# Kernel tuning notes

Hardware: AMD Instinct MI355X
Metric: run time of the kernel (lower is better)

## Reference

```python
import jax, jax.numpy as jnp
import numpy as np

B, C, H, W = 16, 256, 96, 96
K = 3
K2 = K * K


def setup_inputs() -> dict:
    key = jax.random.key(0)
    ks = jax.random.split(key, 8)
    s = 1.0 / np.sqrt(C)  # fan-in style scale for 1x1 convs
    sk = 1.0 / np.sqrt(K2)
    return {
        "x": jax.random.normal(ks[0], (B, C, H, W), jnp.float32),
        "w_xproj": jax.random.normal(ks[1], (C, C), jnp.float32) * s,
        "b_xproj": jnp.zeros((C,), jnp.float32),
        "w_proj": jax.random.normal(ks[2], (C, C), jnp.float32) * s,
        "b_proj": jnp.zeros((C,), jnp.float32),
        "w_kp": jax.random.normal(ks[3], (C, C), jnp.float32) * s,
        "b_kp": jnp.zeros((C,), jnp.float32),
        "w_kg": jax.random.normal(ks[4], (K2, K2), jnp.float32) * sk,
        "b_kg": jnp.zeros((K2,), jnp.float32),
        "diff_ctrl": jnp.zeros((1, 1, 1, C), jnp.float32),
    }


def reference(x, w_xproj, b_xproj, w_proj, b_proj, w_kp, b_kp, w_kg, b_kg, diff_ctrl):
    b, c, h, w = x.shape
    # --- kernel synthesis ---
    # 1x1 conv (kernel_proj)
    kp = jnp.einsum('bchw,oc->bohw', x, w_kp) + b_kp[None, :, None, None]
    # AdaptiveAvgPool1d over flattened spatial dim -> 9 bins (H*W divisible by 9)
    pooled = kp.reshape(b, c, K2, (h * w) // K2).mean(axis=-1)  # [B, C, 9]
    pooled = jax.nn.gelu(pooled)
    # per-channel Linear(9 -> 9): y = W @ v + b
    ker = jnp.einsum('bck,jk->bcj', pooled, w_kg) + b_kg  # [B, C, 9]
    # rearrange 'c (k1 k2) -> k1 k2 1 c' (batched)
    ker = ker.reshape(b, c, K, K).transpose(0, 2, 3, 1)[:, :, :, None, :]  # [B, K, K, 1, C]
    # lateral inhibition: subtract learned fraction of per-channel kernel mean
    factor = jax.nn.sigmoid(diff_ctrl)  # [1, 1, 1, C]
    ker = ker - factor * ker.mean(axis=(1, 2, 3), keepdims=True)
    # --- main path ---
    xp = jnp.einsum('bchw,oc->bohw', x, w_xproj) + b_xproj[None, :, None, None]
    pad = K // 2

    def dwconv(xi, ki):  # xi [C,H,W], ki [K,K,1,C]
        return jax.lax.conv_general_dilated(
            xi[None], ki, window_strides=(1, 1),
            padding=((pad, pad), (pad, pad)),
            dimension_numbers=('NCHW', 'HWIO', 'NCHW'),
            feature_group_count=c)[0]

    y = jax.vmap(dwconv)(xp, ker)  # per-sample dynamic depthwise conv
    out = jnp.einsum('bchw,oc->bohw', y, w_proj) + b_proj[None, :, None, None]
    return out
```

## Files before the change

### kernel.cpp

```cpp
#include <hip/hip_runtime.h>

#define CCH 256
#define HWP 9216
#define IMGDIM 96

typedef __attribute__((ext_vector_type(8))) short s16x8;
typedef __attribute__((ext_vector_type(4))) float f32x4;

__device__ __forceinline__ unsigned short f2bf(float f){
  unsigned u = __float_as_uint(f);
  u += 0x7fffu + ((u >> 16) & 1u);
  return (unsigned short)(u >> 16);
}
__device__ __forceinline__ float bf2f(unsigned short h){
  return __uint_as_float(((unsigned)h) << 16);
}

__global__ void k0_convert(const float* __restrict__ wx, const float* __restrict__ wp,
                           unsigned short* __restrict__ wxb, unsigned short* __restrict__ wpb){
  int i = blockIdx.x * 256 + threadIdx.x;
  wxb[i] = f2bf(wx[i]);
  wpb[i] = f2bf(wp[i]);
}

__device__ __forceinline__ void wload(const unsigned short* __restrict__ wbf,
                                      int obase, int c0, int g, int r, s16x8 wf[8]){
  #pragma unroll
  for (int kk = 0; kk < 2; ++kk){
    #pragma unroll
    for (int mf = 0; mf < 4; ++mf)
      wf[kk*4+mf] = *(const s16x8*)(wbf + (size_t)(obase + mf*16 + r)*CCH + c0 + kk*32 + g*8);
  }
}
__device__ __forceinline__ void gemm_chunk_w(const unsigned short* buf, const s16x8 wf[8],
                                             f32x4 acc[4][4], int g, int r){
  #pragma unroll
  for (int kk = 0; kk < 2; ++kk){
    const int kc = kk*32 + g*8;
    s16x8 bfr[4];
    #pragma unroll
    for (int nf = 0; nf < 4; ++nf){
      const int p = nf*16 + r;
      unsigned off = (unsigned)(p*128 + kc*2) ^ ((unsigned)(p & 7) << 4);
      bfr[nf] = *(const s16x8*)((const char*)buf + off);
    }
    #pragma unroll
    for (int mf = 0; mf < 4; ++mf){
      #pragma unroll
      for (int nf = 0; nf < 4; ++nf){
        acc[mf][nf] = __builtin_amdgcn_mfma_f32_16x16x32_bf16(wf[kk*4+mf], bfr[nf], acc[mf][nf], 0, 0, 0);
      }
    }
  }
}

__device__ __forceinline__ void k1_load(const float* __restrict__ xb, int p0, int c0,
                                        int pg, int cgl, float v[4][4]){
  #pragma unroll
  for (int ci = 0; ci < 4; ++ci){
    float4 q = *(const float4*)(xb + (size_t)(c0 + cgl*4 + ci)*HWP + p0 + pg*4);
    v[ci][0]=q.x; v[ci][1]=q.y; v[ci][2]=q.z; v[ci][3]=q.w;
  }
}
__device__ __forceinline__ void k1_store(unsigned short* buf, int pg, int cgl, float v[4][4],
                                         float* __restrict__ xpart, int c0, int lane, int bbase){
  #pragma unroll
  for (int pj = 0; pj < 4; ++pj){
    const int p = pg*4 + pj;
    unsigned off = (unsigned)(p*128 + cgl*8) ^ ((unsigned)(p & 7) << 4);
    ushort4 pk;
    pk.x = f2bf(v[0][pj]); pk.y = f2bf(v[1][pj]);
    pk.z = f2bf(v[2][pj]); pk.w = f2bf(v[3][pj]);
    *(ushort4*)((char*)buf + off) = pk;
  }
  #pragma unroll
  for (int ci = 0; ci < 4; ++ci){
    float s = v[ci][0] + v[ci][1] + v[ci][2] + v[ci][3];
    s += __shfl_xor(s, 1); s += __shfl_xor(s, 2);
    s += __shfl_xor(s, 4); s += __shfl_xor(s, 8);
    if ((lane & 15) == 0) xpart[bbase + c0 + cgl*4 + ci] = s;
  }
}

__global__ __launch_bounds__(256) void k1_xproj(const float* __restrict__ x,
    const unsigned short* __restrict__ wxb, const float* __restrict__ bx,
    unsigned short* __restrict__ xp, float* __restrict__ xpart){
  const int tile = blockIdx.x, b = blockIdx.y;
  const int p0 = tile * 64;
  const int t = threadIdx.x, lane = t & 63, wave = t >> 6;
  const int g = lane >> 4, r = lane & 15;
  __shared__ __align__(16) unsigned short xlds[2][64*64];

  const float* xb = x + (size_t)b * CCH * HWP;
  const int binj = p0 >> 10, blk = (p0 >> 6) & 15;
  const int bbase = (((int)b*9 + binj)*16 + blk)*CCH;
  const int pg = t & 15, cgl = t >> 4;

  float v[4][4][4];
  s16x8 wf[2][8];
  f32x4 acc[4][4];
  f32x4 zz = {0.f,0.f,0.f,0.f};
  #pragma unroll
  for (int i2=0;i2<4;++i2){
    #pragma unroll
    for (int j2=0;j2<4;++j2) acc[i2][j2] = zz;
  }

  #pragma unroll
  for (int ch = 0; ch < 4; ++ch) k1_load(xb, p0, ch*64, pg, cgl, v[ch]);
  wload(wxb, wave*64, 0, g, r, wf[0]);
  k1_store(xlds[0], pg, cgl, v[0], xpart, 0, lane, bbase);

  #pragma unroll
  for (int ch = 0; ch < 4; ++ch){
    __syncthreads();
    if (ch < 3) wload(wxb, wave*64, (ch+1)*64, g, r, wf[(ch+1)&1]);
    gemm_chunk_w(xlds[ch & 1], wf[ch & 1], acc, g, r);
    if (ch < 3) k1_store(xlds[(ch+1)&1], pg, cgl, v[ch+1], xpart, (ch+1)*64, lane, bbase);
  }

  unsigned short* eb = &xlds[0][0];
  #pragma unroll
  for (int h = 0; h < 2; ++h){
    __syncthreads();
    if ((wave >> 1) == h){
      const int mw = wave & 1;
      #pragma unroll
      for (int mf = 0; mf < 4; ++mf){
        const int o  = mw*64 + mf*16 + 4*g;
        const int og = h*128 + o;
        float b0 = bx[og], b1 = bx[og+1], b2 = bx[og+2], b3 = bx[og+3];
        #pragma unroll
        for (int nf = 0; nf < 4; ++nf){
          const int p = nf*16 + r;
          unsigned off = (unsigned)(p*256 + o*2) ^ ((unsigned)(p & 7) << 4);
          ushort4 pk;
          pk.x = f2bf(acc[mf][nf][0] + b0);
          pk.y = f2bf(acc[mf][nf][1] + b1);
          pk.z = f2bf(acc[mf][nf][2] + b2);
          pk.w = f2bf(acc[mf][nf][3] + b3);
          *(ushort4*)((char*)eb + off) = pk;
        }
      }
    }
    __syncthreads();
    const size_t gb = ((size_t)b*HWP + p0)*CCH + h*128;
    #pragma unroll
    for (int it = 0; it < 4; ++it){
      const unsigned u = it*256 + t;
      const unsigned p = u >> 4, unit = u & 15;
      const unsigned srcoff = (u*16u) ^ ((p & 7) << 4);
      uint4 val = *(const uint4*)((const char*)eb + srcoff);
      *(uint4*)(xp + gb + (size_t)p*CCH + unit*8) = val;
    }
  }
}

__global__ __launch_bounds__(256) void k2a_pooled(const float* __restrict__ xpart,
    const float* __restrict__ wkp, const float* __restrict__ bkp,
    float* __restrict__ pooledg){
  const int j = blockIdx.x, b = blockIdx.y, t = threadIdx.x;
  __shared__ float xbar[256];
  __shared__ float wch[256][65];
  const float* xp0 = xpart + (((size_t)b*9 + j)*16)*CCH;
  float s = 0.f;
  #pragma unroll
  for (int blk = 0; blk < 16; ++blk) s += xp0[blk*CCH + t];
  xbar[t] = s * (1.0f/1024.0f);
  float acc = bkp[t];
  for (int ch = 0; ch < 4; ++ch){
    __syncthreads();
    for (int u = t; u < 256*64; u += 256){
      wch[u >> 6][u & 63] = wkp[(size_t)(u >> 6)*CCH + ch*64 + (u & 63)];
    }
    __syncthreads();
    #pragma unroll
    for (int c = 0; c < 64; ++c) acc += wch[t][c] * xbar[ch*64 + c];
  }
  float x3 = acc*acc*acc;
  float tg = tanhf(0.7978845608028654f*(acc + 0.044715f*x3));
  pooledg[((size_t)b*9 + j)*CCH + t] = 0.5f*acc*(1.0f + tg);
}

__global__ void k2b_ker(const float* __restrict__ pooledg, const float* __restrict__ wkg,
                        const float* __restrict__ bkg, const float* __restrict__ dctrl,
                        float* __restrict__ kerg){
  const int b = blockIdx.x, c = threadIdx.x;
  float pl[9];
  #pragma unroll
  for (int k = 0; k < 9; ++k) pl[k] = pooledg[((size_t)b*9 + k)*CCH + c];
  float kv[9]; float m = 0.f;
  #pragma unroll
  for (int jp = 0; jp < 9; ++jp){
    float s2 = bkg[jp];
    #pragma unroll
    for (int k = 0; k < 9; ++k) s2 += pl[k] * wkg[jp*9 + k];
    kv[jp] = s2; m += s2;
  }
  m *= (1.0f/9.0f);
  float f = 1.0f / (1.0f + expf(-dctrl[c]));
  #pragma unroll
  for (int jp = 0; jp < 9; ++jp) kerg[((size_t)b*9 + jp)*CCH + c] = kv[jp] - f*m;
}

__global__ __launch_bounds__(256) void k3f_conv(const unsigned short* __restrict__ xp,
    const unsigned short* __restrict__ wpb, const float* __restrict__ bp,
    const float* __restrict__ kerg, float* __restrict__ out){
  const int tile = blockIdx.x, b = blockIdx.y;
  const int th0 = (tile / 12) * 8, tw0 = (tile % 12) * 8;
  const int t = threadIdx.x, lane = t & 63, wave = t >> 6;
  const int g = lane >> 4, r = lane & 15;
  __shared__ __align__(16) unsigned short halo[2][100*64];
  __shared__ __align__(16) unsigned short ylds[2][64*64];
  __shared__ __align__(16) float kl[9][256];

  for (int u = t; u < 9*256; u += 256)
    kl[u >> 8][u & 255] = kerg[((size_t)b*9 + (u >> 8))*CCH + (u & 255)];

  const unsigned short* xpb = xp + (size_t)b * HWP * CCH;
  const int p = t >> 2, dh = p >> 3, dw = p & 7, q = t & 3;

  uint4 sreg[4];
  s16x8 wf[2][8];
  f32x4 acc[4][4];
  f32x4 zz = {0.f,0.f,0.f,0.f};
  #pragma unroll
  for (int i2=0;i2<4;++i2){
    #pragma unroll
    for (int j2=0;j2<4;++j2) acc[i2][j2] = zz;
  }

  #define K3F_ISSUE(CH)                                                        \
    _Pragma("unroll")                                                          \
    for (int i = 0; i < 4; ++i){                                               \
      const int u = i*256 + t;                                                 \
      if (u < 800){                                                            \
        const int pos = u >> 3, w8 = u & 7;                                    \
        const int rr = pos / 10, cc = pos % 10;                                \
        const int hh = th0 + rr - 1, ww = tw0 + cc - 1;                        \
        uint4 val = {0u,0u,0u,0u};                                             \
        if (hh >= 0 && hh < IMGDIM && ww >= 0 && ww < IMGDIM)                  \
          val = *(const uint4*)(xpb + ((size_t)(hh*IMGDIM + ww))*CCH + (CH)*64 + w8*8); \
        sreg[i] = val;                                                         \
      }                                                                        \
    }
  #define K3F_WRITE(BUF)                                                       \
    _Pragma("unroll")                                                          \
    for (int i = 0; i < 4; ++i){                                               \
      const int u = i*256 + t;                                                 \
      if (u < 800){                                                            \
        const int pos = u >> 3, w8 = u & 7;                                    \
        unsigned off = (unsigned)(pos*128 + w8*16) ^ ((unsigned)(pos & 7) << 4); \
        *(uint4*)((char*)halo[BUF] + off) = sreg[i];                           \
      }                                                                        \
    }

  wload(wpb, wave*64, 0, g, r, wf[0]);
  K3F_ISSUE(0)
  K3F_WRITE(0)
  __syncthreads();

  #pragma unroll
  for (int ch = 0; ch < 4; ++ch){
    if (ch < 3) K3F_ISSUE(ch+1)
    if (ch > 0) gemm_chunk_w(ylds[(ch-1)&1], wf[(ch-1)&1], acc, g, r);
    if (ch < 3) wload(wpb, wave*64, (ch+1)*64, g, r, wf[(ch+1)&1]);
    #pragma unroll
    for (int ci = 0; ci < 2; ++ci){
      const int c = q*16 + ci*8;
      const int cg = ch*64 + c;
      float a8[8] = {0,0,0,0,0,0,0,0};
      #pragma unroll
      for (int tap = 0; tap < 9; ++tap){
        const int pos = (dh + tap/3)*10 + (dw + tap%3);
        unsigned hof = (unsigned)(pos*128 + c*2) ^ ((unsigned)(pos & 7) << 4);
        union { uint4 qv; unsigned short u16[8]; } hv;
        hv.qv = *(const uint4*)((const char*)halo[ch & 1] + hof);
        const float4* kp4 = (const float4*)&kl[tap][cg];
        float4 ka = kp4[0], kb = kp4[1];
        a8[0] += bf2f(hv.u16[0]) * ka.x;
        a8[1] += bf2f(hv.u16[1]) * ka.y;
        a8[2] += bf2f(hv.u16[2]) * ka.z;
        a8[3] += bf2f(hv.u16[3]) * ka.w;
        a8[4] += bf2f(hv.u16[4]) * kb.x;
        a8[5] += bf2f(hv.u16[5]) * kb.y;
        a8[6] += bf2f(hv.u16[6]) * kb.z;
        a8[7] += bf2f(hv.u16[7]) * kb.w;
      }
      unsigned pk[4];
      #pragma unroll
      for (int e = 0; e < 4; ++e)
        pk[e] = (unsigned)f2bf(a8[2*e]) | ((unsigned)f2bf(a8[2*e+1]) << 16);
      unsigned yoff = (unsigned)(p*128 + c*2) ^ ((unsigned)(p & 7) << 4);
      *(uint4*)((char*)ylds[ch & 1] + yoff) = *(uint4*)pk;
    }
    if (ch < 3) K3F_WRITE((ch+1)&1)
    __syncthreads();
  }
  #undef K3F_ISSUE
  #undef K3F_WRITE

  gemm_chunk_w(ylds[1], wf[1], acc, g, r);

  #pragma unroll
  for (int mf = 0; mf < 4; ++mf){
    const int o = wave*64 + mf*16 + 4*g;
    float b0 = bp[o], b1 = bp[o+1], b2 = bp[o+2], b3 = bp[o+3];
    #pragma unroll
    for (int nf = 0; nf < 4; ++nf){
      const int pl2 = nf*16 + r;
      const int hh = th0 + (pl2 >> 3), ww = tw0 + (pl2 & 7);
      const size_t pix = (size_t)hh*IMGDIM + ww;
      out[((size_t)b*CCH + o + 0)*HWP + pix] = acc[mf][nf][0] + b0;
      out[((size_t)b*CCH + o + 1)*HWP + pix] = acc[mf][nf][1] + b1;
      out[((size_t)b*CCH + o + 2)*HWP + pix] = acc[mf][nf][2] + b2;
      out[((size_t)b*CCH + o + 3)*HWP + pix] = acc[mf][nf][3] + b3;
    }
  }
}

extern "C" void kernel_launch(void* const* d_in, const int* in_sizes, int n_in,
                              void* d_out, int out_size, void* d_ws, size_t ws_size,
                              hipStream_t stream){
  const float* x   = (const float*)d_in[0];
  const float* wxp = (const float*)d_in[1];
  const float* bxp = (const float*)d_in[2];
  const float* wpr = (const float*)d_in[3];
  const float* bpr = (const float*)d_in[4];
  const float* wkp = (const float*)d_in[5];
  const float* bkp = (const float*)d_in[6];
  const float* wkg = (const float*)d_in[7];
  const float* bkg = (const float*)d_in[8];
  const float* dct = (const float*)d_in[9];

  char* ws = (char*)d_ws;
  unsigned short* wxb   = (unsigned short*)(ws + 0);
  unsigned short* wpb   = (unsigned short*)(ws + 131072);
  float*          xpart = (float*)(ws + 262144);
  float*          pooled= (float*)(ws + 2621440);
  float*          kerg  = (float*)(ws + 2768896);
  unsigned short* xp    = (unsigned short*)(ws + 2916352);
  float* o = (float*)d_out;

  k0_convert<<<256, 256, 0, stream>>>(wxp, wpr, wxb, wpb);
  k1_xproj<<<dim3(144,16), 256, 0, stream>>>(x, wxb, bxp, xp, xpart);
  k2a_pooled<<<dim3(9,16), 256, 0, stream>>>(xpart, wkp, bkp, pooled);
  k2b_ker<<<16, 256, 0, stream>>>(pooled, wkg, bkg, dct, kerg);
  k3f_conv<<<dim3(144,16), 256, 0, stream>>>(xp, wpb, bpr, kerg, o);
}
```

Before: 280.8 us.

## Cut register and LDS pressure in xproj and conv kernels for higher occupancy

```diff
diff --git a/kernel.cpp b/kernel.cpp
--- a/kernel.cpp
+++ b/kernel.cpp
@@ -1,4 +1,5 @@
 #include <hip/hip_runtime.h>
+#include <hip/hip_bf16.h>
 
 #define CCH 256
 #define HWP 9216
@@ -8,9 +9,8 @@
 typedef __attribute__((ext_vector_type(4))) float f32x4;
 
 __device__ __forceinline__ unsigned short f2bf(float f){
-  unsigned u = __float_as_uint(f);
-  u += 0x7fffu + ((u >> 16) & 1u);
-  return (unsigned short)(u >> 16);
+  __hip_bfloat16 h = __float2bfloat16(f);
+  return *reinterpret_cast<unsigned short*>(&h);
 }
 __device__ __forceinline__ float bf2f(unsigned short h){
   return __uint_as_float(((unsigned)h) << 16);
@@ -23,21 +23,14 @@
   wpb[i] = f2bf(wp[i]);
 }
 
-__device__ __forceinline__ void wload(const unsigned short* __restrict__ wbf,
-                                      int obase, int c0, int g, int r, s16x8 wf[8]){
-  #pragma unroll
-  for (int kk = 0; kk < 2; ++kk){
-    #pragma unroll
-    for (int mf = 0; mf < 4; ++mf)
-      wf[kk*4+mf] = *(const s16x8*)(wbf + (size_t)(obase + mf*16 + r)*CCH + c0 + kk*32 + g*8);
-  }
-}
-__device__ __forceinline__ void gemm_chunk_w(const unsigned short* buf, const s16x8 wf[8],
-                                             f32x4 acc[4][4], int g, int r){
+__device__ __forceinline__ void gemm_chunk(const unsigned short* __restrict__ wbf,
+                                           const unsigned short* buf,
+                                           f32x4 acc[4][4], int lane, int obase, int c0){
+  const int g = lane >> 4, r = lane & 15;
   #pragma unroll
   for (int kk = 0; kk < 2; ++kk){
     const int kc = kk*32 + g*8;
-    s16x8 bfr[4];
+    s16x8 afr[4], bfr[4];
     #pragma unroll
     for (int nf = 0; nf < 4; ++nf){
       const int p = nf*16 + r;
@@ -45,10 +38,13 @@
       bfr[nf] = *(const s16x8*)((const char*)buf + off);
     }
     #pragma unroll
+    for (int mf = 0; mf < 4; ++mf)
+      afr[mf] = *(const s16x8*)(wbf + (size_t)(obase + mf*16 + r)*CCH + c0 + kc);
+    #pragma unroll
     for (int mf = 0; mf < 4; ++mf){
       #pragma unroll
       for (int nf = 0; nf < 4; ++nf){
-        acc[mf][nf] = __builtin_amdgcn_mfma_f32_16x16x32_bf16(wf[kk*4+mf], bfr[nf], acc[mf][nf], 0, 0, 0);
+        acc[mf][nf] = __builtin_amdgcn_mfma_f32_16x16x32_bf16(afr[mf], bfr[nf], acc[mf][nf], 0, 0, 0);
       }
     }
   }
@@ -88,7 +84,6 @@
   const int tile = blockIdx.x, b = blockIdx.y;
   const int p0 = tile * 64;
   const int t = threadIdx.x, lane = t & 63, wave = t >> 6;
-  const int g = lane >> 4, r = lane & 15;
   __shared__ __align__(16) unsigned short xlds[2][64*64];
 
   const float* xb = x + (size_t)b * CCH * HWP;
@@ -96,8 +91,7 @@
   const int bbase = (((int)b*9 + binj)*16 + blk)*CCH;
   const int pg = t & 15, cgl = t >> 4;
 
-  float v[4][4][4];
-  s16x8 wf[2][8];
+  float v[2][4][4];
   f32x4 acc[4][4];
   f32x4 zz = {0.f,0.f,0.f,0.f};
   #pragma unroll
@@ -106,20 +100,19 @@
     for (int j2=0;j2<4;++j2) acc[i2][j2] = zz;
   }
 
-  #pragma unroll
-  for (int ch = 0; ch < 4; ++ch) k1_load(xb, p0, ch*64, pg, cgl, v[ch]);
-  wload(wxb, wave*64, 0, g, r, wf[0]);
+  k1_load(xb, p0, 0, pg, cgl, v[0]);
   k1_store(xlds[0], pg, cgl, v[0], xpart, 0, lane, bbase);
 
   #pragma unroll
   for (int ch = 0; ch < 4; ++ch){
     __syncthreads();
-    if (ch < 3) wload(wxb, wave*64, (ch+1)*64, g, r, wf[(ch+1)&1]);
-    gemm_chunk_w(xlds[ch & 1], wf[ch & 1], acc, g, r);
-    if (ch < 3) k1_store(xlds[(ch+1)&1], pg, cgl, v[ch+1], xpart, (ch+1)*64, lane, bbase);
+    if (ch < 3) k1_load(xb, p0, (ch+1)*64, pg, cgl, v[(ch+1)&1]);
+    gemm_chunk(wxb, xlds[ch & 1], acc, lane, wave*64, ch*64);
+    if (ch < 3) k1_store(xlds[(ch+1)&1], pg, cgl, v[(ch+1)&1], xpart, (ch+1)*64, lane, bbase);
   }
 
   unsigned short* eb = &xlds[0][0];
+  const int g = lane >> 4, r = lane & 15;
   #pragma unroll
   for (int h = 0; h < 2; ++h){
     __syncthreads();
@@ -203,14 +196,14 @@
   for (int jp = 0; jp < 9; ++jp) kerg[((size_t)b*9 + jp)*CCH + c] = kv[jp] - f*m;
 }
 
-__global__ __launch_bounds__(256) void k3f_conv(const unsigned short* __restrict__ xp,
+__global__ __launch_bounds__(256, 4) void k3g_conv(const unsigned short* __restrict__ xp,
     const unsigned short* __restrict__ wpb, const float* __restrict__ bp,
     const float* __restrict__ kerg, float* __restrict__ out){
-  const int tile = blockIdx.x, b = blockIdx.y;
+  const int bx = blockIdx.x, b = blockIdx.y;
+  const int tile = (bx & 7)*18 + (bx >> 3);
   const int th0 = (tile / 12) * 8, tw0 = (tile % 12) * 8;
   const int t = threadIdx.x, lane = t & 63, wave = t >> 6;
-  const int g = lane >> 4, r = lane & 15;
-  __shared__ __align__(16) unsigned short halo[2][100*64];
+  __shared__ __align__(16) unsigned short halo[100*64];
   __shared__ __align__(16) unsigned short ylds[2][64*64];
   __shared__ __align__(16) float kl[9][256];
 
@@ -221,7 +214,6 @@
   const int p = t >> 2, dh = p >> 3, dw = p & 7, q = t & 3;
 
   uint4 sreg[4];
-  s16x8 wf[2][8];
   f32x4 acc[4][4];
   f32x4 zz = {0.f,0.f,0.f,0.f};
   #pragma unroll
@@ -230,7 +222,7 @@
     for (int j2=0;j2<4;++j2) acc[i2][j2] = zz;
   }
 
-  #define K3F_ISSUE(CH)                                                        \
+  #define K3G_ISSUE(CH)                                                        \
     _Pragma("unroll")                                                          \
     for (int i = 0; i < 4; ++i){                                               \
       const int u = i*256 + t;                                                 \
@@ -244,64 +236,69 @@
         sreg[i] = val;                                                         \
       }                                                                        \
     }
-  #define K3F_WRITE(BUF)                                                       \
+  #define K3G_WRITE()                                                         \
     _Pragma("unroll")                                                          \
     for (int i = 0; i < 4; ++i){                                               \
       const int u = i*256 + t;                                                 \
       if (u < 800){                                                            \
         const int pos = u >> 3, w8 = u & 7;                                    \
         unsigned off = (unsigned)(pos*128 + w8*16) ^ ((unsigned)(pos & 7) << 4); \
-        *(uint4*)((char*)halo[BUF] + off) = sreg[i];                           \
+        *(uint4*)((char*)halo + off) = sreg[i];                                \
       }                                                                        \
     }
-
-  wload(wpb, wave*64, 0, g, r, wf[0]);
-  K3F_ISSUE(0)
-  K3F_WRITE(0)
+  #define K3G_CONV(CH)                                                        \
+    _Pragma("unroll")                                                          \
+    for (int ci = 0; ci < 2; ++ci){                                            \
+      const int c = q*16 + ci*8;                                               \
+      const int cg = (CH)*64 + c;                                              \
+      float a8[8] = {0,0,0,0,0,0,0,0};                                         \
+      _Pragma("unroll")                                                        \
+      for (int tap = 0; tap < 9; ++tap){                                       \
+        const int pos = (dh + tap/3)*10 + (dw + tap%3);                        \
+        unsigned hof = (unsigned)(pos*128 + c*2) ^ ((unsigned)(pos & 7) << 4); \
+        union { uint4 qv; unsigned short u16[8]; } hv;                         \
+        hv.qv = *(const uint4*)((const char*)halo + hof);                      \
+        const float4* kp4 = (const float4*)&kl[tap][cg];                       \
+        float4 ka = kp4[0], kb = kp4[1];                                       \
+        a8[0] += bf2f(hv.u16[0]) * ka.x;                                       \
+        a8[1] += bf2f(hv.u16[1]) * ka.y;                                       \
+        a8[2] += bf2f(hv.u16[2]) * ka.z;                                       \
+        a8[3] += bf2f(hv.u16[3]) * ka.w;                                       \
+        a8[4] += bf2f(hv.u16[4]) * kb.x;                                       \
+        a8[5] += bf2f(hv.u16[5]) * kb.y;                                       \
+        a8[6] += bf2f(hv.u16[6]) * kb.z;                                       \
+        a8[7] += bf2f(hv.u16[7]) * kb.w;                                       \
+      }                                                                        \
+      unsigned pk[4];                                                          \
+      _Pragma("unroll")                                                        \
+      for (int e = 0; e < 4; ++e)                                              \
+        pk[e] = (unsigned)f2bf(a8[2*e]) | ((unsigned)f2bf(a8[2*e+1]) << 16);   \
+      unsigned yoff = (unsigned)(p*128 + c*2) ^ ((unsigned)(p & 7) << 4);      \
+      *(uint4*)((char*)ylds[(CH) & 1] + yoff) = *(uint4*)pk;                   \
+    }
+
+  K3G_ISSUE(0)
+  K3G_WRITE()
   __syncthreads();
-
-  #pragma unroll
-  for (int ch = 0; ch < 4; ++ch){
-    if (ch < 3) K3F_ISSUE(ch+1)
-    if (ch > 0) gemm_chunk_w(ylds[(ch-1)&1], wf[(ch-1)&1], acc, g, r);
-    if (ch < 3) wload(wpb, wave*64, (ch+1)*64, g, r, wf[(ch+1)&1]);
-    #pragma unroll
-    for (int ci = 0; ci < 2; ++ci){
-      const int c = q*16 + ci*8;
-      const int cg = ch*64 + c;
-      float a8[8] = {0,0,0,0,0,0,0,0};
-      #pragma unroll
-      for (int tap = 0; tap < 9; ++tap){
-        const int pos = (dh + tap/3)*10 + (dw + tap%3);
-        unsigned hof = (unsigned)(pos*128 + c*2) ^ ((unsigned)(pos & 7) << 4);
-        union { uint4 qv; unsigned short u16[8]; } hv;
-        hv.qv = *(const uint4*)((const char*)halo[ch & 1] + hof);
-        const float4* kp4 = (const float4*)&kl[tap][cg];
-        float4 ka = kp4[0], kb = kp4[1];
-        a8[0] += bf2f(hv.u16[0]) * ka.x;
-        a8[1] += bf2f(hv.u16[1]) * ka.y;
-        a8[2] += bf2f(hv.u16[2]) * ka.z;
-        a8[3] += bf2f(hv.u16[3]) * ka.w;
-        a8[4] += bf2f(hv.u16[4]) * kb.x;
-        a8[5] += bf2f(hv.u16[5]) * kb.y;
-        a8[6] += bf2f(hv.u16[6]) * kb.z;
-        a8[7] += bf2f(hv.u16[7]) * kb.w;
-      }
-      unsigned pk[4];
-      #pragma unroll
-      for (int e = 0; e < 4; ++e)
-        pk[e] = (unsigned)f2bf(a8[2*e]) | ((unsigned)f2bf(a8[2*e+1]) << 16);
-      unsigned yoff = (unsigned)(p*128 + c*2) ^ ((unsigned)(p & 7) << 4);
-      *(uint4*)((char*)ylds[ch & 1] + yoff) = *(uint4*)pk;
-    }
-    if (ch < 3) K3F_WRITE((ch+1)&1)
-    __syncthreads();
-  }
-  #undef K3F_ISSUE
-  #undef K3F_WRITE
-
-  gemm_chunk_w(ylds[1], wf[1], acc, g, r);
-
+  K3G_CONV(0)
+  __syncthreads();
+
+  #pragma unroll
+  for (int ch = 1; ch < 4; ++ch){
+    K3G_ISSUE(ch)
+    gemm_chunk(wpb, ylds[(ch-1)&1], acc, lane, wave*64, (ch-1)*64);
+    K3G_WRITE()
+    __syncthreads();
+    K3G_CONV(ch)
+    __syncthreads();
+  }
+  #undef K3G_ISSUE
+  #undef K3G_WRITE
+  #undef K3G_CONV
+
+  gemm_chunk(wpb, ylds[1], acc, lane, wave*64, 192);
+
+  const int g = lane >> 4, r = lane & 15;
   #pragma unroll
   for (int mf = 0; mf < 4; ++mf){
     const int o = wave*64 + mf*16 + 4*g;
@@ -346,5 +343,5 @@
   k1_xproj<<<dim3(144,16), 256, 0, stream>>>(x, wxb, bxp, xp, xpart);
   k2a_pooled<<<dim3(9,16), 256, 0, stream>>>(xpart, wkp, bkp, pooled);
   k2b_ker<<<16, 256, 0, stream>>>(pooled, wkg, bkg, dct, kerg);
-  k3f_conv<<<dim3(144,16), 256, 0, stream>>>(xp, wpb, bpr, kerg, o);
-}
+  k3g_conv<<<dim3(144,16), 256, 0, stream>>>(xp, wpb, bpr, kerg, o);
+}
```

Measured after the change: 357.6 us. +27.3%, slower.
